# Kernel optimization log

Hardware: AMD Instinct MI355X
Metric: run time of the kernel (lower is better)

Reference implementation:

```python
import jax, jax.numpy as jnp
import numpy as np

B, ORDER, N, D, H = 16, 2, 512, 128, 8
DH = D // H
NEG_SLOPE = 0.2


def setup_inputs() -> dict:
    key = jax.random.key(0)
    ks = jax.random.split(key, 8)
    stdv = 1.0 / np.sqrt(DH)

    def u(k, shape):
        return jax.random.uniform(k, shape, jnp.float32, -stdv, stdv)

    x = jax.random.normal(ks[0], (B, ORDER, N, D), jnp.float32)
    A = jax.random.randint(ks[1], (B, ORDER, N, N), 0, 5, jnp.int32)
    # Stacked params for the 2*order GAT modules: axis0 = order, axis1 = (conv1, conv2)
    W = u(ks[2], (ORDER, 2, D, D))            # project.weight
    pb = jnp.zeros((ORDER, 2, D), jnp.float32)  # project.bias (init 0)
    att_src = u(ks[3], (ORDER, 2, H, DH))
    att_dst = u(ks[4], (ORDER, 2, H, DH))
    bias = jnp.zeros((ORDER, 2, D), jnp.float32)  # GAT output bias (init 0)
    return {"x": x, "A": A, "W": W, "pb": pb,
            "att_src": att_src, "att_dst": att_dst, "bias": bias}


def _gat(x, Af, W, pb, a_src, a_dst, b):
    # x: [B,N,D]; Af: [B,N,N] float in {0,1}
    xp = x @ W.T + pb                                  # project
    xh = xp.reshape(B, N, H, DH)                       # [B,N,H,DH]
    s_src = jnp.einsum('bnhd,hd->bnh', xh, a_src)      # [B,N,H]
    s_dst = jnp.einsum('bnhd,hd->bnh', xh, a_dst)
    alpha = s_src[:, :, None, :] + s_dst[:, None, :, :]  # [B,src,dst,H]
    alpha = jnp.where((Af != 1.0)[..., None], 0.0, alpha)
    alpha = jnp.where(alpha >= 0, alpha, NEG_SLOPE * alpha)  # leaky relu
    alpha = jax.nn.softmax(alpha, axis=1)              # softmax over src dim
    out = jnp.einsum('bsdh,bshf->bdhf', alpha, xh).reshape(B, N, D)
    out = out + xp                                     # add_self_loops
    return out + b


def reference(x, A, W, pb, att_src, att_dst, bias):
    A1 = ((A == 2) | (A == 4)).astype(x.dtype)  # [B,ORDER,N,N]
    A2 = ((A == 3) | (A == 4)).astype(x.dtype)
    hs = []
    for i in range(ORDER):
        h1 = _gat(x[:, i], A1[:, i], W[i, 0], pb[i, 0], att_src[i, 0], att_dst[i, 0], bias[i, 0])
        h2 = _gat(x[:, i], A2[:, i], W[i, 1], pb[i, 1], att_src[i, 1], att_dst[i, 1], bias[i, 1])
        hs.append(h1 + h2)
    h = jnp.stack(hs, axis=1)                          # [B,ORDER,N,D]
    out = h + h.mean(axis=1, keepdims=True)
    return out
```

## Files before the change

### kernel.cpp

```cpp
#include <hip/hip_runtime.h>

#define N_ 512
#define D_ 128
#define LOG2E 1.44269504088896f


typedef __attribute__((ext_vector_type(8))) short short8;
typedef __attribute__((ext_vector_type(4))) float floatx4;
typedef __attribute__((ext_vector_type(4))) unsigned int uintx4;

#if defined(__has_builtin)
#if __has_builtin(__builtin_amdgcn_exp2f)
#define EXP2F(x) __builtin_amdgcn_exp2f(x)
#else
#define EXP2F(x) exp2f(x)
#endif
#else
#define EXP2F(x) exp2f(x)
#endif

__device__ __forceinline__ unsigned short f2bf(float f) {
    unsigned int u = __float_as_uint(f);
    u += 0x7fffu + ((u >> 16) & 1u);
    return (unsigned short)(u >> 16);
}
__device__ __forceinline__ float bflo(unsigned int u) { return __uint_as_float(u << 16); }
__device__ __forceinline__ float bfhi(unsigned int u) { return __uint_as_float(u & 0xffff0000u); }

__global__ __launch_bounds__(256) void maskprep_kernel(
    const int* __restrict__ A, unsigned short* __restrict__ mg)
{
    const int bid = blockIdx.x;
    const int stile = bid & 31;
    const int bi = bid >> 5;
    const int t = threadIdx.x;
    const int sl = t >> 4, lane = t & 15;
    const int s = stile * 16 + sl;
    const int* Ar = A + ((size_t)bi * N_ + s) * N_ + lane * 32;
    unsigned int m0 = 0, m1 = 0;
#pragma unroll
    for (int g = 0; g < 8; ++g) {
        const int4 v = *(const int4*)(Ar + g * 4);
        const int k = g * 4;
        if (v.x == 2 || v.x == 4) m0 |= 1u << (k + 0);
        if (v.x == 3 || v.x == 4) m1 |= 1u << (k + 0);
        if (v.y == 2 || v.y == 4) m0 |= 1u << (k + 1);
        if (v.y == 3 || v.y == 4) m1 |= 1u << (k + 1);
        if (v.z == 2 || v.z == 4) m0 |= 1u << (k + 2);
        if (v.z == 3 || v.z == 4) m1 |= 1u << (k + 2);
        if (v.w == 2 || v.w == 4) m0 |= 1u << (k + 3);
        if (v.w == 3 || v.w == 4) m1 |= 1u << (k + 3);
    }
    const size_t b0 = ((size_t)bi * 2 + 0) * 32 * N_;
    const size_t b1 = ((size_t)bi * 2 + 1) * 32 * N_;
    const int T0 = lane * 2, T1 = lane * 2 + 1;
    mg[b0 + (size_t)T0 * N_ + s] = (unsigned short)(m0 & 0xFFFFu);
    mg[b0 + (size_t)T1 * N_ + s] = (unsigned short)(m0 >> 16);
    mg[b1 + (size_t)T0 * N_ + s] = (unsigned short)(m1 & 0xFFFFu);
    mg[b1 + (size_t)T1 * N_ + s] = (unsigned short)(m1 >> 16);
}

__global__ __launch_bounds__(256) void proj_kernel(
    const float* __restrict__ x, const float* __restrict__ W,
    const float* __restrict__ pb, const float* __restrict__ att_src,
    const float* __restrict__ att_dst,
    unsigned short* __restrict__ xpt, float* __restrict__ sg)
{
    const int bid = blockIdx.x;
    const int unit = bid >> 1;
    const int half = bid & 1;
    const int ntile = unit & 7;
    const int inst  = unit >> 3;
    const int j = inst & 1;
    const int bi = inst >> 1;
    const int ij = (bi & 1) * 2 + j;
    const int t = threadIdx.x;
    const int wave = t >> 6, L = t & 63, n = L & 15, q = L >> 4;

    const int n0w = ntile * 64 + wave * 16;
    const float* xrow = x + ((size_t)bi * N_ + n0w + n) * D_ + q * 8;
    short8 Af[4];
#pragma unroll
    for (int kc = 0; kc < 4; ++kc) {
        const float4 a0 = *(const float4*)(xrow + kc * 32);
        const float4 a1 = *(const float4*)(xrow + kc * 32 + 4);
        uintx4 au;
        au.x = f2bf(a0.x) | ((unsigned int)f2bf(a0.y) << 16);
        au.y = f2bf(a0.z) | ((unsigned int)f2bf(a0.w) << 16);
        au.z = f2bf(a1.x) | ((unsigned int)f2bf(a1.y) << 16);
        au.w = f2bf(a1.z) | ((unsigned int)f2bf(a1.w) << 16);
        Af[kc] = __builtin_bit_cast(short8, au);
    }

    const float* wb = W + (size_t)ij * D_ * D_;
#pragma unroll
    for (int ft = 0; ft < 4; ++ft) {
        const int head = half * 4 + ft;
        const int fg = head * 16 + n;
        const float* wrow = wb + (size_t)fg * D_ + q * 8;
        floatx4 C = (floatx4){0.f, 0.f, 0.f, 0.f};
#pragma unroll
        for (int kc = 0; kc < 4; ++kc) {
            const float4 b0 = *(const float4*)(wrow + kc * 32);
            const float4 b1 = *(const float4*)(wrow + kc * 32 + 4);
            uintx4 bu;
            bu.x = f2bf(b0.x) | ((unsigned int)f2bf(b0.y) << 16);
            bu.y = f2bf(b0.z) | ((unsigned int)f2bf(b0.w) << 16);
            bu.z = f2bf(b1.x) | ((unsigned int)f2bf(b1.y) << 16);
            bu.w = f2bf(b1.z) | ((unsigned int)f2bf(b1.w) << 16);
            C = __builtin_amdgcn_mfma_f32_16x16x32_bf16(
                Af[kc], __builtin_bit_cast(short8, bu), C, 0, 0, 0);
        }
        const float pbv = pb[ij * D_ + fg];
        float xp0 = C[0] + pbv, xp1 = C[1] + pbv;
        float xp2 = C[2] + pbv, xp3 = C[3] + pbv;
        uint2 pk;
        pk.x = f2bf(xp0) | ((unsigned int)f2bf(xp1) << 16);
        pk.y = f2bf(xp2) | ((unsigned int)f2bf(xp3) << 16);
        *(uint2*)&xpt[((size_t)inst * D_ + fg) * N_ + n0w + q * 4] = pk;

        const float asv = att_src[ij * D_ + fg];
        const float adv = att_dst[ij * D_ + fg];
        float sa0 = xp0 * asv, sa1 = xp1 * asv, sa2 = xp2 * asv, sa3 = xp3 * asv;
        float sb0 = xp0 * adv, sb1 = xp1 * adv, sb2 = xp2 * adv, sb3 = xp3 * adv;
#pragma unroll
        for (int off = 1; off < 16; off <<= 1) {
            sa0 += __shfl_xor(sa0, off); sa1 += __shfl_xor(sa1, off);
            sa2 += __shfl_xor(sa2, off); sa3 += __shfl_xor(sa3, off);
            sb0 += __shfl_xor(sb0, off); sb1 += __shfl_xor(sb1, off);
            sb2 += __shfl_xor(sb2, off); sb3 += __shfl_xor(sb3, off);
        }
        if (n < 4) {
            const float v = (n == 0) ? sa0 : (n == 1) ? sa1 : (n == 2) ? sa2 : sa3;
            sg[(((size_t)inst * 2 + 0) * 8 + head) * N_ + n0w + q * 4 + n] = v * LOG2E;
        } else if (n >= 8 && n < 12) {
            const int r = n - 8;
            const float v = (r == 0) ? sb0 : (r == 1) ? sb1 : (r == 2) ? sb2 : sb3;
            sg[(((size_t)inst * 2 + 1) * 8 + head) * N_ + n0w + q * 4 + r] = v * LOG2E;
        }
    }
}

__global__ __launch_bounds__(256) void attn_kernel(
    const unsigned short* __restrict__ xpt,
    const float* __restrict__ sg,
    const unsigned short* __restrict__ mg,
    const float* __restrict__ bias,
    float* __restrict__ hout)
{
    __shared__ float ss_l[8 * N_];
    __shared__ unsigned short mask_l[N_];

    const int bid = blockIdx.x;
    const int tile = bid & 31;
    const int cj   = (bid >> 5) & 1;
    const int bi   = bid >> 6;
    const int inst = bi * 2 + cj;
    const int ij = (bi & 1) * 2 + cj;
    const int d0 = tile * 16;
    const int t = threadIdx.x;
    const int wave = t >> 6, L = t & 63, n = L & 15, q = L >> 4;
    const int h0 = wave * 2;
    const int n16 = n + 16;

    {
        const float4* src = (const float4*)(sg + (size_t)inst * 2 * 8 * N_);
        float4* dst = (float4*)ss_l;
#pragma unroll
        for (int r = 0; r < 4; ++r) dst[r * 256 + t] = src[r * 256 + t];
    }
    if (t < 64)
        ((uint4*)mask_l)[t] =
            ((const uint4*)(mg + ((size_t)inst * 32 + tile) * N_))[t];

    float sdv[2];
#pragma unroll
    for (int hh = 0; hh < 2; ++hh)
        sdv[hh] = sg[(((size_t)inst * 2 + 1) * 8 + h0 + hh) * N_ + d0 + n];

    __syncthreads();

    const unsigned short* xpi = xpt + (size_t)inst * D_ * N_;

    const uintx4 ou = { 0x3F803F80u, 0x3F803F80u, 0x3F803F80u, 0x3F803F80u };
    const short8 onesB = __builtin_bit_cast(short8, ou);

    floatx4 Cacc[2] = { (floatx4){0.f,0.f,0.f,0.f}, (floatx4){0.f,0.f,0.f,0.f} };
    floatx4 Cz[2]   = { (floatx4){0.f,0.f,0.f,0.f}, (floatx4){0.f,0.f,0.f,0.f} };

    short8 Bf0 = *(const short8*)(xpi + (size_t)(h0 * 16 + n) * N_ + q * 8);
    short8 Bf1 = *(const short8*)(xpi + (size_t)((h0 + 1) * 16 + n) * N_ + q * 8);
    for (int c = 0; c < 16; ++c) {
        const int sq = c * 32 + q * 8;
        short8 nB0, nB1;
        if (c < 15) {
            nB0 = *(const short8*)(xpi + (size_t)(h0 * 16 + n) * N_ + sq + 32);
            nB1 = *(const short8*)(xpi + (size_t)((h0 + 1) * 16 + n) * N_ + sq + 32);
        }
        const uint4 mv = *(const uint4*)&mask_l[sq];
        const unsigned int mw[4] = { mv.x, mv.y, mv.z, mv.w };
#pragma unroll
        for (int hh = 0; hh < 2; ++hh) {
            const float4 s0v = *(const float4*)&ss_l[(h0 + hh) * N_ + sq];
            const float4 s1v = *(const float4*)&ss_l[(h0 + hh) * N_ + sq + 4];
            const float ssv[8] = { s0v.x, s0v.y, s0v.z, s0v.w,
                                   s1v.x, s1v.y, s1v.z, s1v.w };
            unsigned int wt[8];
#pragma unroll
            for (int idx = 0; idx < 8; ++idx) {
                const float z0 = ssv[idx] + sdv[hh];
                const float zr = fmaxf(z0, 0.2f * z0);
                const float e = EXP2F(zr);
                const unsigned int bit =
                    (mw[idx >> 1] >> ((idx & 1) ? n16 : n)) & 1u;
                wt[idx] = __float_as_uint(bit ? e : 1.0f);
            }
            uintx4 au;
            au.x = __builtin_amdgcn_perm(wt[1], wt[0], 0x07060302);
            au.y = __builtin_amdgcn_perm(wt[3], wt[2], 0x07060302);
            au.z = __builtin_amdgcn_perm(wt[5], wt[4], 0x07060302);
            au.w = __builtin_amdgcn_perm(wt[7], wt[6], 0x07060302);
            const short8 As = __builtin_bit_cast(short8, au);
            Cacc[hh] = __builtin_amdgcn_mfma_f32_16x16x32_bf16(
                As, hh ? Bf1 : Bf0, Cacc[hh], 0, 0, 0);
            Cz[hh] = __builtin_amdgcn_mfma_f32_16x16x32_bf16(
                As, onesB, Cz[hh], 0, 0, 0);
        }
        Bf0 = nB0;
        Bf1 = nB1;
    }

#pragma unroll
    for (int hh = 0; hh < 2; ++hh) {
        const int h = h0 + hh;
        const float bv = bias[ij * D_ + h * 16 + n];
        const uint2 sv = *(const uint2*)(xpi + (size_t)(h * 16 + n) * N_ + d0 + q * 4);
        const float selfv[4] = { bflo(sv.x), bfhi(sv.x), bflo(sv.y), bfhi(sv.y) };
#pragma unroll
        for (int reg = 0; reg < 4; ++reg) {
            const float Zi = 1.0f / Cz[hh][reg];
            const float val = Cacc[hh][reg] * Zi + selfv[reg] + bv;
            unsafeAtomicAdd(
                &hout[((size_t)bi * N_ + d0 + q * 4 + reg) * D_ + h * 16 + n], val);
        }
    }
}

__global__ __launch_bounds__(256) void combine_kernel(float* __restrict__ h)
{
    const int idx = blockIdx.x * 256 + threadIdx.x;
    const int b = idx >> 14;
    const int r = idx & 16383;
    float4* p0 = (float4*)h + (size_t)b * 32768 + r;
    float4* p1 = p0 + 16384;
    const float4 a = *p0;
    const float4 o = *p1;
    float4 r0, r1;
    r0.x = 1.5f * a.x + 0.5f * o.x;  r1.x = 1.5f * o.x + 0.5f * a.x;
    r0.y = 1.5f * a.y + 0.5f * o.y;  r1.y = 1.5f * o.y + 0.5f * a.y;
    r0.z = 1.5f * a.z + 0.5f * o.z;  r1.z = 1.5f * o.z + 0.5f * a.z;
    r0.w = 1.5f * a.w + 0.5f * o.w;  r1.w = 1.5f * o.w + 0.5f * a.w;
    *p0 = r0;
    *p1 = r1;
}

extern "C" void kernel_launch(void* const* d_in, const int* in_sizes, int n_in,
                              void* d_out, int out_size, void* d_ws, size_t ws_size,
                              hipStream_t stream)
{
    const float* x   = (const float*)d_in[0];
    const int*   A   = (const int*)d_in[1];
    const float* W   = (const float*)d_in[2];
    const float* pb  = (const float*)d_in[3];
    const float* as_ = (const float*)d_in[4];
    const float* ad_ = (const float*)d_in[5];
    const float* bs  = (const float*)d_in[6];

    unsigned short* xpt = (unsigned short*)d_ws;
    float* sg = (float*)(xpt + (size_t)64 * D_ * N_);
    unsigned short* mg = (unsigned short*)(sg + (size_t)64 * 2 * 8 * N_);
    float* h = (float*)d_out;

    hipMemsetAsync(d_out, 0, (size_t)out_size * sizeof(float), stream);
    maskprep_kernel<<<1024, 256, 0, stream>>>(A, mg);
    proj_kernel<<<1024, 256, 0, stream>>>(x, W, pb, as_, ad_, xpt, sg);
    attn_kernel<<<2048, 256, 0, stream>>>(xpt, sg, mg, bs, h);
    combine_kernel<<<1024, 256, 0, stream>>>(h);
}
```

Baseline: 164.9 us.

## Factor leaky-relu exp into precomputed per-node exponentials and merge prep kernels

Merges the mask-prep and projection kernels into one launch by dispatching on block index. It also precomputes exp2 of each source score and of its 0.2-scaled value, packs both as bf16, and stores per-destination exp2 values. The attention inner loop then forms the weight as a max of products, scaled by the inverse destination exponential, instead of calling exp per element. This removes transcendental work from the hot loop at the cost of bf16 rounding of the exponentials and possible overflow or underflow for large scores.

```diff
diff --git a/kernel.cpp b/kernel.cpp
--- a/kernel.cpp
+++ b/kernel.cpp
@@ -27,54 +27,54 @@
 __device__ __forceinline__ float bflo(unsigned int u) { return __uint_as_float(u << 16); }
 __device__ __forceinline__ float bfhi(unsigned int u) { return __uint_as_float(u & 0xffff0000u); }
 
-__global__ __launch_bounds__(256) void maskprep_kernel(
-    const int* __restrict__ A, unsigned short* __restrict__ mg)
-{
-    const int bid = blockIdx.x;
-    const int stile = bid & 31;
-    const int bi = bid >> 5;
-    const int t = threadIdx.x;
-    const int sl = t >> 4, lane = t & 15;
-    const int s = stile * 16 + sl;
-    const int* Ar = A + ((size_t)bi * N_ + s) * N_ + lane * 32;
-    unsigned int m0 = 0, m1 = 0;
-#pragma unroll
-    for (int g = 0; g < 8; ++g) {
-        const int4 v = *(const int4*)(Ar + g * 4);
-        const int k = g * 4;
-        if (v.x == 2 || v.x == 4) m0 |= 1u << (k + 0);
-        if (v.x == 3 || v.x == 4) m1 |= 1u << (k + 0);
-        if (v.y == 2 || v.y == 4) m0 |= 1u << (k + 1);
-        if (v.y == 3 || v.y == 4) m1 |= 1u << (k + 1);
-        if (v.z == 2 || v.z == 4) m0 |= 1u << (k + 2);
-        if (v.z == 3 || v.z == 4) m1 |= 1u << (k + 2);
-        if (v.w == 2 || v.w == 4) m0 |= 1u << (k + 3);
-        if (v.w == 3 || v.w == 4) m1 |= 1u << (k + 3);
-    }
-    const size_t b0 = ((size_t)bi * 2 + 0) * 32 * N_;
-    const size_t b1 = ((size_t)bi * 2 + 1) * 32 * N_;
-    const int T0 = lane * 2, T1 = lane * 2 + 1;
-    mg[b0 + (size_t)T0 * N_ + s] = (unsigned short)(m0 & 0xFFFFu);
-    mg[b0 + (size_t)T1 * N_ + s] = (unsigned short)(m0 >> 16);
-    mg[b1 + (size_t)T0 * N_ + s] = (unsigned short)(m1 & 0xFFFFu);
-    mg[b1 + (size_t)T1 * N_ + s] = (unsigned short)(m1 >> 16);
-}
-
-__global__ __launch_bounds__(256) void proj_kernel(
+__global__ __launch_bounds__(256) void prep_kernel(
     const float* __restrict__ x, const float* __restrict__ W,
     const float* __restrict__ pb, const float* __restrict__ att_src,
-    const float* __restrict__ att_dst,
-    unsigned short* __restrict__ xpt, float* __restrict__ sg)
-{
-    const int bid = blockIdx.x;
-    const int unit = bid >> 1;
-    const int half = bid & 1;
+    const float* __restrict__ att_dst, const int* __restrict__ A,
+    unsigned short* __restrict__ xpt, unsigned int* __restrict__ sgE,
+    float2* __restrict__ sgD, unsigned short* __restrict__ mg)
+{
+    const int bid0 = blockIdx.x;
+    const int t = threadIdx.x;
+
+    if (bid0 >= 1024) {
+        const int bid = bid0 - 1024;
+        const int stile = bid & 31;
+        const int bi = bid >> 5;
+        const int sl = t >> 4, lane = t & 15;
+        const int s = stile * 16 + sl;
+        const int* Ar = A + ((size_t)bi * N_ + s) * N_ + lane * 32;
+        unsigned int m0 = 0, m1 = 0;
+#pragma unroll
+        for (int g = 0; g < 8; ++g) {
+            const int4 v = *(const int4*)(Ar + g * 4);
+            const int k = g * 4;
+            if (v.x == 2 || v.x == 4) m0 |= 1u << (k + 0);
+            if (v.x == 3 || v.x == 4) m1 |= 1u << (k + 0);
+            if (v.y == 2 || v.y == 4) m0 |= 1u << (k + 1);
+            if (v.y == 3 || v.y == 4) m1 |= 1u << (k + 1);
+            if (v.z == 2 || v.z == 4) m0 |= 1u << (k + 2);
+            if (v.z == 3 || v.z == 4) m1 |= 1u << (k + 2);
+            if (v.w == 2 || v.w == 4) m0 |= 1u << (k + 3);
+            if (v.w == 3 || v.w == 4) m1 |= 1u << (k + 3);
+        }
+        const size_t b0 = ((size_t)bi * 2 + 0) * 32 * N_;
+        const size_t b1 = ((size_t)bi * 2 + 1) * 32 * N_;
+        const int T0 = lane * 2, T1 = lane * 2 + 1;
+        mg[b0 + (size_t)T0 * N_ + s] = (unsigned short)(m0 & 0xFFFFu);
+        mg[b0 + (size_t)T1 * N_ + s] = (unsigned short)(m0 >> 16);
+        mg[b1 + (size_t)T0 * N_ + s] = (unsigned short)(m1 & 0xFFFFu);
+        mg[b1 + (size_t)T1 * N_ + s] = (unsigned short)(m1 >> 16);
+        return;
+    }
+
+    const int unit = bid0 >> 1;
+    const int half = bid0 & 1;
     const int ntile = unit & 7;
     const int inst  = unit >> 3;
     const int j = inst & 1;
     const int bi = inst >> 1;
     const int ij = (bi & 1) * 2 + j;
-    const int t = threadIdx.x;
     const int wave = t >> 6, L = t & 63, n = L & 15, q = L >> 4;
 
     const int n0w = ntile * 64 + wave * 16;
@@ -131,24 +131,30 @@
             sb2 += __shfl_xor(sb2, off); sb3 += __shfl_xor(sb3, off);
         }
         if (n < 4) {
-            const float v = (n == 0) ? sa0 : (n == 1) ? sa1 : (n == 2) ? sa2 : sa3;
-            sg[(((size_t)inst * 2 + 0) * 8 + head) * N_ + n0w + q * 4 + n] = v * LOG2E;
+            const float v = ((n == 0) ? sa0 : (n == 1) ? sa1 : (n == 2) ? sa2 : sa3) * LOG2E;
+            const unsigned int pkv = f2bf(EXP2F(v)) |
+                ((unsigned int)f2bf(EXP2F(0.2f * v)) << 16);
+            sgE[((size_t)inst * 8 + head) * N_ + n0w + q * 4 + n] = pkv;
         } else if (n >= 8 && n < 12) {
             const int r = n - 8;
-            const float v = (r == 0) ? sb0 : (r == 1) ? sb1 : (r == 2) ? sb2 : sb3;
-            sg[(((size_t)inst * 2 + 1) * 8 + head) * N_ + n0w + q * 4 + r] = v * LOG2E;
+            const float v = ((r == 0) ? sb0 : (r == 1) ? sb1 : (r == 2) ? sb2 : sb3) * LOG2E;
+            float2 ed;
+            ed.x = EXP2F(v);
+            ed.y = EXP2F(0.2f * v);
+            sgD[((size_t)inst * 8 + head) * N_ + n0w + q * 4 + r] = ed;
         }
     }
 }
 
 __global__ __launch_bounds__(256) void attn_kernel(
     const unsigned short* __restrict__ xpt,
-    const float* __restrict__ sg,
+    const unsigned int* __restrict__ sgE,
+    const float2* __restrict__ sgD,
     const unsigned short* __restrict__ mg,
     const float* __restrict__ bias,
     float* __restrict__ hout)
 {
-    __shared__ float ss_l[8 * N_];
+    __shared__ unsigned int es_l[8 * N_];
     __shared__ unsigned short mask_l[N_];
 
     const int bid = blockIdx.x;
@@ -164,8 +170,8 @@
     const int n16 = n + 16;
 
     {
-        const float4* src = (const float4*)(sg + (size_t)inst * 2 * 8 * N_);
-        float4* dst = (float4*)ss_l;
+        const uint4* src = (const uint4*)(sgE + (size_t)inst * 8 * N_);
+        uint4* dst = (uint4*)es_l;
 #pragma unroll
         for (int r = 0; r < 4; ++r) dst[r * 256 + t] = src[r * 256 + t];
     }
@@ -173,10 +179,13 @@
         ((uint4*)mask_l)[t] =
             ((const uint4*)(mg + ((size_t)inst * 32 + tile) * N_))[t];
 
-    float sdv[2];
-#pragma unroll
-    for (int hh = 0; hh < 2; ++hh)
-        sdv[hh] = sg[(((size_t)inst * 2 + 1) * 8 + h0 + hh) * N_ + d0 + n];
+    float iEd[2], rd[2];
+#pragma unroll
+    for (int hh = 0; hh < 2; ++hh) {
+        const float2 ed = sgD[((size_t)inst * 8 + h0 + hh) * N_ + d0 + n];
+        iEd[hh] = 1.0f / ed.x;
+        rd[hh] = ed.y * iEd[hh];
+    }
 
     __syncthreads();
 
@@ -201,19 +210,19 @@
         const unsigned int mw[4] = { mv.x, mv.y, mv.z, mv.w };
 #pragma unroll
         for (int hh = 0; hh < 2; ++hh) {
-            const float4 s0v = *(const float4*)&ss_l[(h0 + hh) * N_ + sq];
-            const float4 s1v = *(const float4*)&ss_l[(h0 + hh) * N_ + sq + 4];
-            const float ssv[8] = { s0v.x, s0v.y, s0v.z, s0v.w,
-                                   s1v.x, s1v.y, s1v.z, s1v.w };
+            const uint4 e0 = *(const uint4*)&es_l[(h0 + hh) * N_ + sq];
+            const uint4 e1 = *(const uint4*)&es_l[(h0 + hh) * N_ + sq + 4];
+            const unsigned int epk[8] = { e0.x, e0.y, e0.z, e0.w,
+                                          e1.x, e1.y, e1.z, e1.w };
             unsigned int wt[8];
 #pragma unroll
             for (int idx = 0; idx < 8; ++idx) {
-                const float z0 = ssv[idx] + sdv[hh];
-                const float zr = fmaxf(z0, 0.2f * z0);
-                const float e = EXP2F(zr);
+                const float Es = bflo(epk[idx]);
+                const float Fs = bfhi(epk[idx]);
+                const float wv = fmaxf(Es, Fs * rd[hh]);
                 const unsigned int bit =
                     (mw[idx >> 1] >> ((idx & 1) ? n16 : n)) & 1u;
-                wt[idx] = __float_as_uint(bit ? e : 1.0f);
+                wt[idx] = __float_as_uint(bit ? wv : iEd[hh]);
             }
             uintx4 au;
             au.x = __builtin_amdgcn_perm(wt[1], wt[0], 0x07060302);
@@ -277,13 +286,13 @@
     const float* bs  = (const float*)d_in[6];
 
     unsigned short* xpt = (unsigned short*)d_ws;
-    float* sg = (float*)(xpt + (size_t)64 * D_ * N_);
-    unsigned short* mg = (unsigned short*)(sg + (size_t)64 * 2 * 8 * N_);
+    unsigned int* sgE = (unsigned int*)(xpt + (size_t)64 * D_ * N_);
+    float2* sgD = (float2*)(sgE + (size_t)64 * 8 * N_);
+    unsigned short* mg = (unsigned short*)(sgD + (size_t)64 * 8 * N_);
     float* h = (float*)d_out;
 
     hipMemsetAsync(d_out, 0, (size_t)out_size * sizeof(float), stream);
-    maskprep_kernel<<<1024, 256, 0, stream>>>(A, mg);
-    proj_kernel<<<1024, 256, 0, stream>>>(x, W, pb, as_, ad_, xpt, sg);
-    attn_kernel<<<2048, 256, 0, stream>>>(xpt, sg, mg, bs, h);
+    prep_kernel<<<2048, 256, 0, stream>>>(x, W, pb, as_, ad_, A, xpt, sgE, sgD, mg);
+    attn_kernel<<<2048, 256, 0, stream>>>(xpt, sgE, sgD, mg, bs, h);
     combine_kernel<<<1024, 256, 0, stream>>>(h);
 }
```

After: 159.5 us. 3.3% less time.
